# Performance work log

Hardware: AMD Instinct MI355X
Metric: run time of the kernel (lower is better)

The kernel has to match this reference:

```python
import jax, jax.numpy as jnp
import numpy as np

E, E2, T, C, H = 500_000, 1_000_000, 1_000_000, 64, 64
EPS, EPS2 = 0.0, 0.0  # train_eps=False, eps=eps2=0.0


def setup_inputs() -> dict:
    key = jax.random.key(0)
    ks = jax.random.split(key, 16)
    s = 1.0 / np.sqrt(C)
    return {
        "edge_attr": jax.random.normal(ks[0], (E, C), jnp.float32),
        "edge_attr2": jax.random.normal(ks[1], (E2, C), jnp.float32),
        # 6 projection layers (C -> C)
        "Wp": jax.random.normal(ks[2], (6, C, C), jnp.float32) * s,
        "bp": jnp.zeros((6, C), jnp.float32),
        # MLP 0 (for 1-hop edges): C -> H -> C
        "W1a": jax.random.normal(ks[3], (C, H), jnp.float32) * s,
        "b1a": jnp.zeros((H,), jnp.float32),
        "W2a": jax.random.normal(ks[4], (H, C), jnp.float32) * (1.0 / np.sqrt(H)),
        "b2a": jnp.zeros((C,), jnp.float32),
        # MLP 1 (for 2-hop edges): C -> H -> C
        "W1b": jax.random.normal(ks[5], (C, H), jnp.float32) * s,
        "b1b": jnp.zeros((H,), jnp.float32),
        "W2b": jax.random.normal(ks[6], (H, C), jnp.float32) * (1.0 / np.sqrt(H)),
        "b2b": jnp.zeros((C,), jnp.float32),
        # triangle index lists [3, T]; all values < E so valid for both edge arrays
        "triangle_1_1_1": jax.random.randint(ks[7], (3, T), 0, E, jnp.int64),
        "triangle_1_1_2": jax.random.randint(ks[8], (3, T), 0, E, jnp.int64),
        "triangle_1_2_2": jax.random.randint(ks[9], (3, T), 0, E, jnp.int64),
        "triangle_2_2_2": jax.random.randint(ks[10], (3, T), 0, E, jnp.int64),
        "inverse_edge_1": jax.random.randint(ks[11], (E,), 0, E, jnp.int64),
        "inverse_edge_2": jax.random.randint(ks[12], (E2,), 0, E, jnp.int64),
    }


def reference(edge_attr, edge_attr2, Wp, bp, W1a, b1a, W2a, b2a,
              W1b, b1b, W2b, b2b,
              triangle_1_1_1, triangle_1_1_2, triangle_1_2_2, triangle_2_2_2,
              inverse_edge_1, inverse_edge_2):
    num_edges = edge_attr.shape[0]
    num_edges2 = edge_attr2.shape[0]

    def proj(i, x):  # Linear proj i applied to gathered-sum features
        return x @ Wp[i] + bp[i]

    def mlp_a(x):
        return jax.nn.relu(x @ W1a + b1a) @ W2a + b2a

    def mlp_b(x):
        return jax.nn.relu(x @ W1b + b1b) @ W2b + b2b

    ij111, ik111, kj111 = triangle_1_1_1
    ij112, ik112, kj112 = triangle_1_1_2
    ij122, ik122, kj122 = triangle_1_2_2
    ij222, ik222, kj222 = triangle_2_2_2

    m111 = jax.ops.segment_sum(proj(0, edge_attr[ik111] + edge_attr[kj111]), ij111, num_segments=num_edges)
    m112 = jax.ops.segment_sum(proj(1, edge_attr[ik112] + edge_attr2[kj112]), ij112, num_segments=num_edges)
    m122 = jax.ops.segment_sum(proj(2, edge_attr2[ik122] + edge_attr2[kj122]), ij122, num_segments=num_edges)
    edge_attr = mlp_a(edge_attr * (1.0 + EPS) + m111 + m112 + m112[inverse_edge_1] + m122)

    m211 = jax.ops.segment_sum(proj(3, edge_attr[ij112] + edge_attr[ik112]), kj112, num_segments=num_edges2)
    m212 = jax.ops.segment_sum(proj(4, edge_attr[ij122] + edge_attr2[kj122]), ik122, num_segments=num_edges2)
    m222 = jax.ops.segment_sum(proj(5, edge_attr2[ik222] + edge_attr2[kj222]), ij222, num_segments=num_edges2)
    edge_attr2 = mlp_b(edge_attr2 * (1.0 + EPS2) + m211 + m212 + m212[inverse_edge_2] + m222)

    return (edge_attr, edge_attr2)
```

## Files before the change

kernel.cpp:

```cpp
#include <hip/hip_runtime.h>

#define CH 64
typedef unsigned int uint;
typedef unsigned short ushort;

typedef __attribute__((ext_vector_type(8))) short bf16x8;
typedef __attribute__((ext_vector_type(4))) float f32x4;

__device__ __forceinline__ float bf_lo(uint u){ union{uint a;float f;}c; c.a=u<<16; return c.f; }
__device__ __forceinline__ float bf_hi(uint u){ union{uint a;float f;}c; c.a=u&0xffff0000u; return c.f; }
__device__ __forceinline__ ushort f2bf(float f){
    uint a = __float_as_uint(f);
    a = (a + 0x7fffu + ((a>>16)&1u)) >> 16;
    return (ushort)a;
}
__device__ __forceinline__ uint pack2(float lo, float hi){
    return (uint)f2bf(lo) | ((uint)f2bf(hi) << 16);
}
__device__ __forceinline__ void atom_pk(uint* addr, float lo, float hi){
    uint v = pack2(lo, hi);
    asm volatile("global_atomic_pk_add_bf16 %0, %1, off" :: "v"(addr), "v"(v) : "memory");
}

template<bool ABF, bool BBF>
__global__ __launch_bounds__(256) void scatter_sum(
    const void* __restrict__ Av, const void* __restrict__ Bv,
    const int* __restrict__ idx_dst, const int* __restrict__ idx_a,
    const int* __restrict__ idx_b, int T,
    uint* __restrict__ S, float* __restrict__ cnt)
{
    const int l32  = threadIdx.x & 31;
    const int half = (threadIdx.x >> 5) & 1;
    const int wave  = blockIdx.x * (blockDim.x >> 6) + (threadIdx.x >> 6);
    const int nwave = gridDim.x * (blockDim.x >> 6);
    for (int w = wave; 2 * w < T; w += nwave) {
        const int t = 2 * w + half;
        if (t >= T) continue;
        const int ia = idx_a[t], ib = idx_b[t], id = idx_dst[t];
        float ax, ay, bx, by;
        if (ABF) { uint u = ((const uint*)Av)[(size_t)ia*32 + l32]; ax = bf_lo(u); ay = bf_hi(u); }
        else     { float2 v = ((const float2*)Av)[(size_t)ia*32 + l32]; ax = v.x; ay = v.y; }
        if (BBF) { uint u = ((const uint*)Bv)[(size_t)ib*32 + l32]; bx = bf_lo(u); by = bf_hi(u); }
        else     { float2 v = ((const float2*)Bv)[(size_t)ib*32 + l32]; bx = v.x; by = v.y; }
        atom_pk(S + (size_t)id*32 + l32, ax+bx, ay+by);
        if (l32 == 0) atomicAdd(&cnt[id], 1.0f);
    }
}

__global__ __launch_bounds__(256) void conv_bf16_kernel(
    const float* __restrict__ src, uint* __restrict__ dst, long n4)
{
    long i = (long)blockIdx.x * blockDim.x + threadIdx.x;
    const long stride = (long)gridDim.x * blockDim.x;
    for (; i < n4; i += stride) {
        const float4 v = ((const float4*)src)[i];
        uint2 o; o.x = pack2(v.x, v.y); o.y = pack2(v.z, v.w);
        ((uint2*)dst)[i] = o;
    }
}

struct W10 { const float* p[10]; };
__global__ __launch_bounds__(256) void prep_weights(W10 srcs, char* __restrict__ img)
{
    const float* W = srcs.p[blockIdx.x];
    char* im = img + (size_t)blockIdx.x * 8192;
    for (int idx = threadIdx.x; idx < 4096; idx += 256) {
        const int k = idx >> 6, col = idx & 63;
        *(ushort*)(im + col*128 + ((2*k) ^ ((col&7)<<4))) = f2bf(W[idx]);
    }
}

template<bool BASEBF>
__global__ __launch_bounds__(256) void fused_finalize_mfma(
    const void* __restrict__ base,
    const uint* __restrict__ SA, const float* __restrict__ cA,
    const uint* __restrict__ SB, const float* __restrict__ cB,
    const uint* __restrict__ SC, const float* __restrict__ cC,
    const int* __restrict__ inv,
    const char* __restrict__ wi0, const char* __restrict__ wi1,
    const char* __restrict__ wi2, const char* __restrict__ wi3,
    const char* __restrict__ wi4,
    const float* __restrict__ bA, const float* __restrict__ bB,
    const float* __restrict__ bC,
    const float* __restrict__ b1, const float* __restrict__ b2,
    int N, float* __restrict__ out, uint* __restrict__ out_bf)
{
    __shared__ __attribute__((aligned(16))) char lds[49152];
    const int tid = threadIdx.x;

    {
        const char* imgs[5] = {wi0, wi1, wi2, wi3, wi4};
        #pragma unroll
        for (int m = 0; m < 5; ++m) {
            const uint4* s = (const uint4*)imgs[m];
            uint4* d = (uint4*)(lds + m*8192);
            #pragma unroll
            for (int i = 0; i < 2; ++i) d[tid + 256*i] = s[tid + 256*i];
        }
    }
    __syncthreads();

    const int w = tid >> 6, lane = tid & 63;
    const int ln = lane & 15, grp = lane >> 4;
    char* zl = lds + 40960 + w * 2048;
    const int swz = (ln & 7) << 4;

    auto ldW = [&](int m, int kc, int ct) {
        const int col = ct*16 + ln;
        return *(const bf16x8*)(lds + m*8192 + col*128 + ((kc*64 + grp*16) ^ ((col&7)<<4)));
    };
    auto ldS = [&](const uint* Srow, int kc) {
        union { uint4 u; bf16x8 h; } c;
        c.u = *(const uint4*)(Srow + kc*16 + grp*4);
        return c.h;
    };
    auto ldZ = [&](int kc) {
        return *(const bf16x8*)(zl + ln*128 + ((kc*64 + grp*16) ^ swz));
    };
    auto stZ = [&](int ct, float v0, float v1, float v2, float v3) {
        uint2 u; u.x = pack2(v0, v1); u.y = pack2(v2, v3);
        *(uint2*)(zl + ln*128 + ((ct*32 + grp*8) ^ swz)) = u;
    };

    const f32x4 z4 = {0.f, 0.f, 0.f, 0.f};

    #pragma unroll 1
    for (int t = 0; t < 4; ++t) {
        const int rr = blockIdx.x * 256 + w * 64 + t * 16 + ln;
        const int ra = rr < N ? rr : N - 1;
        const bool valid = rr < N;
        const int iv = inv[ra];
        const float fA = cA[ra], fB = cB[ra], fC = cC[ra] + cC[iv];

        const uint* SArow  = SA + (size_t)ra * 32;
        const uint* SBrow  = SB + (size_t)ra * 32;
        const uint* SCrow  = SC + (size_t)ra * 32;
        const uint* SCrow2 = SC + (size_t)iv * 32;

        f32x4 acc[4] = {z4, z4, z4, z4};
        #pragma unroll
        for (int kc = 0; kc < 2; ++kc) {
            const bf16x8 sA = ldS(SArow, kc);
            const bf16x8 sB = ldS(SBrow, kc);
            const bf16x8 sC = ldS(SCrow, kc);
            const bf16x8 sD = ldS(SCrow2, kc);
            #pragma unroll
            for (int ct = 0; ct < 4; ++ct) {
                const bf16x8 wC = ldW(2, kc, ct);
                acc[ct] = __builtin_amdgcn_mfma_f32_16x16x32_bf16(ldW(0,kc,ct), sA, acc[ct], 0,0,0);
                acc[ct] = __builtin_amdgcn_mfma_f32_16x16x32_bf16(ldW(1,kc,ct), sB, acc[ct], 0,0,0);
                acc[ct] = __builtin_amdgcn_mfma_f32_16x16x32_bf16(wC,          sC, acc[ct], 0,0,0);
                acc[ct] = __builtin_amdgcn_mfma_f32_16x16x32_bf16(wC,          sD, acc[ct], 0,0,0);
            }
        }

        #pragma unroll
        for (int ct = 0; ct < 4; ++ct) {
            const int cb = ct*16 + grp*4;
            const float4 vA = *(const float4*)(bA + cb);
            const float4 vB = *(const float4*)(bB + cb);
            const float4 vC = *(const float4*)(bC + cb);
            float e0, e1, e2, e3;
            if (BASEBF) {
                const uint2 u = *(const uint2*)((const uint*)base + (size_t)ra*32 + (cb>>1));
                e0 = bf_lo(u.x); e1 = bf_hi(u.x); e2 = bf_lo(u.y); e3 = bf_hi(u.y);
            } else {
                const float4 b4 = *(const float4*)((const float*)base + (size_t)ra*64 + cb);
                e0 = b4.x; e1 = b4.y; e2 = b4.z; e3 = b4.w;
            }
            stZ(ct,
                acc[ct][0] + e0 + fA*vA.x + fB*vB.x + fC*vC.x,
                acc[ct][1] + e1 + fA*vA.y + fB*vB.y + fC*vC.y,
                acc[ct][2] + e2 + fA*vA.z + fB*vB.z + fC*vC.z,
                acc[ct][3] + e3 + fA*vA.w + fB*vB.w + fC*vC.w);
        }

        f32x4 hacc[4] = {z4, z4, z4, z4};
        #pragma unroll
        for (int kc = 0; kc < 2; ++kc) {
            const bf16x8 zf = ldZ(kc);
            #pragma unroll
            for (int ct = 0; ct < 4; ++ct)
                hacc[ct] = __builtin_amdgcn_mfma_f32_16x16x32_bf16(ldW(3,kc,ct), zf, hacc[ct], 0,0,0);
        }
        #pragma unroll
        for (int ct = 0; ct < 4; ++ct) {
            const int cb = ct*16 + grp*4;
            const float4 v1 = *(const float4*)(b1 + cb);
            stZ(ct, fmaxf(hacc[ct][0] + v1.x, 0.f), fmaxf(hacc[ct][1] + v1.y, 0.f),
                    fmaxf(hacc[ct][2] + v1.z, 0.f), fmaxf(hacc[ct][3] + v1.w, 0.f));
        }

        f32x4 oacc[4] = {z4, z4, z4, z4};
        #pragma unroll
        for (int kc = 0; kc < 2; ++kc) {
            const bf16x8 hf = ldZ(kc);
            #pragma unroll
            for (int ct = 0; ct < 4; ++ct)
                oacc[ct] = __builtin_amdgcn_mfma_f32_16x16x32_bf16(ldW(4,kc,ct), hf, oacc[ct], 0,0,0);
        }
        #pragma unroll
        for (int ct = 0; ct < 4; ++ct) {
            const int cb = ct*16 + grp*4;
            const float4 v2 = *(const float4*)(b2 + cb);
            const float o0 = oacc[ct][0] + v2.x, o1 = oacc[ct][1] + v2.y;
            const float o2 = oacc[ct][2] + v2.z, o3 = oacc[ct][3] + v2.w;
            if (valid) {
                *(float4*)(out + (size_t)ra*64 + cb) = make_float4(o0, o1, o2, o3);
                if (out_bf) {
                    uint2 u; u.x = pack2(o0, o1); u.y = pack2(o2, o3);
                    *(uint2*)(out_bf + (size_t)ra*32 + (cb>>1)) = u;
                }
            }
        }
    }
}

extern "C" void kernel_launch(void* const* d_in, const int* in_sizes, int n_in,
                              void* d_out, int out_size, void* d_ws, size_t ws_size,
                              hipStream_t stream)
{
    const float* ea  = (const float*)d_in[0];
    const float* ea2 = (const float*)d_in[1];
    const float* Wp  = (const float*)d_in[2];
    const float* bp  = (const float*)d_in[3];
    const float* W1a = (const float*)d_in[4];
    const float* b1a = (const float*)d_in[5];
    const float* W2a = (const float*)d_in[6];
    const float* b2a = (const float*)d_in[7];
    const float* W1b = (const float*)d_in[8];
    const float* b1b = (const float*)d_in[9];
    const float* W2b = (const float*)d_in[10];
    const float* b2b = (const float*)d_in[11];
    const int* t111 = (const int*)d_in[12];
    const int* t112 = (const int*)d_in[13];
    const int* t122 = (const int*)d_in[14];
    const int* t222 = (const int*)d_in[15];
    const int* inv1 = (const int*)d_in[16];
    const int* inv2 = (const int*)d_in[17];

    const int E    = in_sizes[0] / CH;
    const int E2   = in_sizes[1] / CH;
    const int T111 = in_sizes[12] / 3;
    const int T112 = in_sizes[13] / 3;
    const int T122 = in_sizes[14] / 3;
    const int T222 = in_sizes[15] / 3;

    float* out1 = (float*)d_out;
    float* out2 = out1 + (size_t)E * CH;

    const size_t R = (size_t)(E > E2 ? E : E2);
    char* p = (char*)d_ws;
    char*  Wimg = p;       p += 10 * 8192;
    uint*  SA = (uint*)p;  p += R * 128;
    uint*  SB = (uint*)p;  p += R * 128;
    uint*  SC = (uint*)p;  p += R * 128;
    float* cA = (float*)p; p += R * 4;
    float* cB = (float*)p; p += R * 4;
    float* cC = (float*)p; p += R * 4;
    size_t used = (size_t)(p - (char*)d_ws);
    uint* ea2_bf = nullptr;
    uint* ea_bf  = nullptr;
    uint* out1_bf = nullptr;
    if (ws_size >= used + (size_t)E2 * 128) { ea2_bf = (uint*)p; p += (size_t)E2 * 128; used += (size_t)E2 * 128; }
    if (ws_size >= used + (size_t)E  * 128) { ea_bf  = (uint*)p; p += (size_t)E  * 128; used += (size_t)E  * 128; }
    if (ws_size >= used + (size_t)E  * 128) { out1_bf = (uint*)p; }

    const dim3 blk256(256);
    const int SCAT_NB = 4096;

    auto scat = [&](const void* A, bool abf, const void* B, bool bbf,
                    const int* dst, const int* ia, const int* ib, int T,
                    uint* S, float* c) {
        if (abf && bbf)
            scatter_sum<true, true ><<<SCAT_NB, blk256, 0, stream>>>(A, B, dst, ia, ib, T, S, c);
        else if (abf)
            scatter_sum<true, false><<<SCAT_NB, blk256, 0, stream>>>(A, B, dst, ia, ib, T, S, c);
        else if (bbf)
            scatter_sum<false, true><<<SCAT_NB, blk256, 0, stream>>>(A, B, dst, ia, ib, T, S, c);
        else
            scatter_sum<false, false><<<SCAT_NB, blk256, 0, stream>>>(A, B, dst, ia, ib, T, S, c);
    };

    W10 w10;
    for (int i = 0; i < 6; ++i) w10.p[i] = Wp + (size_t)i * CH * CH;
    w10.p[6] = W1a; w10.p[7] = W2a; w10.p[8] = W1b; w10.p[9] = W2b;
    prep_weights<<<10, blk256, 0, stream>>>(w10, Wimg);

    if (ea2_bf) conv_bf16_kernel<<<2048, blk256, 0, stream>>>(ea2, ea2_bf, (long)E2 * 16);
    if (ea_bf)  conv_bf16_kernel<<<2048, blk256, 0, stream>>>(ea,  ea_bf,  (long)E  * 16);

    const void* eaS  = ea_bf  ? (const void*)ea_bf  : (const void*)ea;
    const void* ea2S = ea2_bf ? (const void*)ea2_bf : (const void*)ea2;
    const bool eaB = ea_bf != nullptr, ea2B = ea2_bf != nullptr;

    hipMemsetAsync(SA, 0, (size_t)E * 128, stream);
    hipMemsetAsync(SB, 0, (size_t)E * 128, stream);
    hipMemsetAsync(SC, 0, (size_t)E * 128, stream);
    hipMemsetAsync(cA, 0, (size_t)E * 4, stream);
    hipMemsetAsync(cB, 0, (size_t)E * 4, stream);
    hipMemsetAsync(cC, 0, (size_t)E * 4, stream);

    scat(eaS, eaB, eaS, eaB, t111 + 0, t111 + T111, t111 + 2*T111, T111, SA, cA);
    scat(ea2S, ea2B, ea2S, ea2B, t122 + 0, t122 + T122, t122 + 2*T122, T122, SB, cB);
    scat(eaS, eaB, ea2S, ea2B, t112 + 0, t112 + T112, t112 + 2*T112, T112, SC, cC);

    {
        const void* base1 = eaB ? (const void*)ea_bf : (const void*)ea;
        const int NB = (E + 255) / 256;
        if (eaB)
            fused_finalize_mfma<true><<<NB, blk256, 0, stream>>>(
                base1, SA, cA, SB, cB, SC, cC, inv1,
                Wimg + 0*8192, Wimg + 2*8192, Wimg + 1*8192, Wimg + 6*8192, Wimg + 7*8192,
                bp + 0*CH, bp + 2*CH, bp + 1*CH, b1a, b2a, E, out1, out1_bf);
        else
            fused_finalize_mfma<false><<<NB, blk256, 0, stream>>>(
                base1, SA, cA, SB, cB, SC, cC, inv1,
                Wimg + 0*8192, Wimg + 2*8192, Wimg + 1*8192, Wimg + 6*8192, Wimg + 7*8192,
                bp + 0*CH, bp + 2*CH, bp + 1*CH, b1a, b2a, E, out1, out1_bf);
    }

    hipMemsetAsync(SA, 0, (size_t)E2 * 128, stream);
    hipMemsetAsync(SB, 0, (size_t)E2 * 128, stream);
    hipMemsetAsync(SC, 0, (size_t)E2 * 128, stream);
    hipMemsetAsync(cA, 0, (size_t)E2 * 4, stream);
    hipMemsetAsync(cB, 0, (size_t)E2 * 4, stream);
    hipMemsetAsync(cC, 0, (size_t)E2 * 4, stream);

    const void* o1S = out1_bf ? (const void*)out1_bf : (const void*)out1;
    const bool o1B = out1_bf != nullptr;

    scat(o1S, o1B, o1S, o1B, t112 + 2*T112, t112 + 0, t112 + T112, T112, SA, cA);
    scat(ea2S, ea2B, ea2S, ea2B, t222 + 0, t222 + T222, t222 + 2*T222, T222, SB, cB);
    scat(o1S, o1B, ea2S, ea2B, t122 + T122, t122 + 0, t122 + 2*T122, T122, SC, cC);

    {
        const void* base2 = ea2B ? (const void*)ea2_bf : (const void*)ea2;
        const int NB = (E2 + 255) / 256;
        if (ea2B)
            fused_finalize_mfma<true><<<NB, blk256, 0, stream>>>(
                base2, SA, cA, SB, cB, SC, cC, inv2,
                Wimg + 3*8192, Wimg + 5*8192, Wimg + 4*8192, Wimg + 8*8192, Wimg + 9*8192,
                bp + 3*CH, bp + 5*CH, bp + 4*CH, b1b, b2b, E2, out2, nullptr);
        else
            fused_finalize_mfma<false><<<NB, blk256, 0, stream>>>(
                base2, SA, cA, SB, cB, SC, cC, inv2,
                Wimg + 3*8192, Wimg + 5*8192, Wimg + 4*8192, Wimg + 8*8192, Wimg + 9*8192,
                bp + 3*CH, bp + 5*CH, bp + 4*CH, b1b, b2b, E2, out2, nullptr);
    }
}
```

Measured before the change: 1.765 ms.

## Split fused finalize into projection-sum and MLP kernels to cut LDS per block

```diff
diff --git a/kernel.cpp b/kernel.cpp
--- a/kernel.cpp
+++ b/kernel.cpp
@@ -71,27 +71,24 @@
 }
 
 template<bool BASEBF>
-__global__ __launch_bounds__(256) void fused_finalize_mfma(
+__global__ __launch_bounds__(256, 4) void proj_sum_mfma(
     const void* __restrict__ base,
     const uint* __restrict__ SA, const float* __restrict__ cA,
     const uint* __restrict__ SB, const float* __restrict__ cB,
     const uint* __restrict__ SC, const float* __restrict__ cC,
     const int* __restrict__ inv,
-    const char* __restrict__ wi0, const char* __restrict__ wi1,
-    const char* __restrict__ wi2, const char* __restrict__ wi3,
-    const char* __restrict__ wi4,
+    const char* __restrict__ wiA, const char* __restrict__ wiB,
+    const char* __restrict__ wiC,
     const float* __restrict__ bA, const float* __restrict__ bB,
     const float* __restrict__ bC,
-    const float* __restrict__ b1, const float* __restrict__ b2,
-    int N, float* __restrict__ out, uint* __restrict__ out_bf)
-{
-    __shared__ __attribute__((aligned(16))) char lds[49152];
+    int N, uint* __restrict__ z)
+{
+    __shared__ __attribute__((aligned(16))) char lds[24576];
     const int tid = threadIdx.x;
-
     {
-        const char* imgs[5] = {wi0, wi1, wi2, wi3, wi4};
-        #pragma unroll
-        for (int m = 0; m < 5; ++m) {
+        const char* imgs[3] = {wiA, wiB, wiC};
+        #pragma unroll
+        for (int m = 0; m < 3; ++m) {
             const uint4* s = (const uint4*)imgs[m];
             uint4* d = (uint4*)(lds + m*8192);
             #pragma unroll
@@ -102,8 +99,6 @@
 
     const int w = tid >> 6, lane = tid & 63;
     const int ln = lane & 15, grp = lane >> 4;
-    char* zl = lds + 40960 + w * 2048;
-    const int swz = (ln & 7) << 4;
 
     auto ldW = [&](int m, int kc, int ct) {
         const int col = ct*16 + ln;
@@ -113,13 +108,6 @@
         union { uint4 u; bf16x8 h; } c;
         c.u = *(const uint4*)(Srow + kc*16 + grp*4);
         return c.h;
-    };
-    auto ldZ = [&](int kc) {
-        return *(const bf16x8*)(zl + ln*128 + ((kc*64 + grp*16) ^ swz));
-    };
-    auto stZ = [&](int ct, float v0, float v1, float v2, float v3) {
-        uint2 u; u.x = pack2(v0, v1); u.y = pack2(v2, v3);
-        *(uint2*)(zl + ln*128 + ((ct*32 + grp*8) ^ swz)) = u;
     };
 
     const f32x4 z4 = {0.f, 0.f, 0.f, 0.f};
@@ -168,36 +156,92 @@
                 const float4 b4 = *(const float4*)((const float*)base + (size_t)ra*64 + cb);
                 e0 = b4.x; e1 = b4.y; e2 = b4.z; e3 = b4.w;
             }
-            stZ(ct,
-                acc[ct][0] + e0 + fA*vA.x + fB*vB.x + fC*vC.x,
-                acc[ct][1] + e1 + fA*vA.y + fB*vB.y + fC*vC.y,
-                acc[ct][2] + e2 + fA*vA.z + fB*vB.z + fC*vC.z,
-                acc[ct][3] + e3 + fA*vA.w + fB*vB.w + fC*vC.w);
-        }
+            if (valid) {
+                uint2 u;
+                u.x = pack2(acc[ct][0] + e0 + fA*vA.x + fB*vB.x + fC*vC.x,
+                            acc[ct][1] + e1 + fA*vA.y + fB*vB.y + fC*vC.y);
+                u.y = pack2(acc[ct][2] + e2 + fA*vA.z + fB*vB.z + fC*vC.z,
+                            acc[ct][3] + e3 + fA*vA.w + fB*vB.w + fC*vC.w);
+                *(uint2*)(z + (size_t)ra*32 + (cb>>1)) = u;
+            }
+        }
+    }
+}
+
+__global__ __launch_bounds__(256, 4) void mlp_mfma(
+    const uint* __restrict__ z,
+    const char* __restrict__ wi1, const char* __restrict__ wi2,
+    const float* __restrict__ b1, const float* __restrict__ b2,
+    int N, float* __restrict__ out, uint* __restrict__ out_bf)
+{
+    __shared__ __attribute__((aligned(16))) char lds[24576];
+    const int tid = threadIdx.x;
+    {
+        const char* imgs[2] = {wi1, wi2};
+        #pragma unroll
+        for (int m = 0; m < 2; ++m) {
+            const uint4* s = (const uint4*)imgs[m];
+            uint4* d = (uint4*)(lds + m*8192);
+            #pragma unroll
+            for (int i = 0; i < 2; ++i) d[tid + 256*i] = s[tid + 256*i];
+        }
+    }
+    __syncthreads();
+
+    const int w = tid >> 6, lane = tid & 63;
+    const int ln = lane & 15, grp = lane >> 4;
+    char* zl = lds + 16384 + w * 2048;
+    const int swz = (ln & 7) << 4;
+
+    auto ldW = [&](int m, int kc, int ct) {
+        const int col = ct*16 + ln;
+        return *(const bf16x8*)(lds + m*8192 + col*128 + ((kc*64 + grp*16) ^ ((col&7)<<4)));
+    };
+    auto ldZg = [&](const uint* zrow, int kc) {
+        union { uint4 u; bf16x8 h; } c;
+        c.u = *(const uint4*)(zrow + kc*16 + grp*4);
+        return c.h;
+    };
+    auto ldZl = [&](int kc) {
+        return *(const bf16x8*)(zl + ln*128 + ((kc*64 + grp*16) ^ swz));
+    };
+    auto stZl = [&](int ct, float v0, float v1, float v2, float v3) {
+        uint2 u; u.x = pack2(v0, v1); u.y = pack2(v2, v3);
+        *(uint2*)(zl + ln*128 + ((ct*32 + grp*8) ^ swz)) = u;
+    };
+
+    const f32x4 z4 = {0.f, 0.f, 0.f, 0.f};
+
+    #pragma unroll 1
+    for (int t = 0; t < 4; ++t) {
+        const int rr = blockIdx.x * 256 + w * 64 + t * 16 + ln;
+        const int ra = rr < N ? rr : N - 1;
+        const bool valid = rr < N;
+        const uint* zrow = z + (size_t)ra * 32;
 
         f32x4 hacc[4] = {z4, z4, z4, z4};
         #pragma unroll
         for (int kc = 0; kc < 2; ++kc) {
-            const bf16x8 zf = ldZ(kc);
+            const bf16x8 zf = ldZg(zrow, kc);
             #pragma unroll
             for (int ct = 0; ct < 4; ++ct)
-                hacc[ct] = __builtin_amdgcn_mfma_f32_16x16x32_bf16(ldW(3,kc,ct), zf, hacc[ct], 0,0,0);
+                hacc[ct] = __builtin_amdgcn_mfma_f32_16x16x32_bf16(ldW(0,kc,ct), zf, hacc[ct], 0,0,0);
         }
         #pragma unroll
         for (int ct = 0; ct < 4; ++ct) {
             const int cb = ct*16 + grp*4;
             const float4 v1 = *(const float4*)(b1 + cb);
-            stZ(ct, fmaxf(hacc[ct][0] + v1.x, 0.f), fmaxf(hacc[ct][1] + v1.y, 0.f),
-                    fmaxf(hacc[ct][2] + v1.z, 0.f), fmaxf(hacc[ct][3] + v1.w, 0.f));
+            stZl(ct, fmaxf(hacc[ct][0] + v1.x, 0.f), fmaxf(hacc[ct][1] + v1.y, 0.f),
+                     fmaxf(hacc[ct][2] + v1.z, 0.f), fmaxf(hacc[ct][3] + v1.w, 0.f));
         }
 
         f32x4 oacc[4] = {z4, z4, z4, z4};
         #pragma unroll
         for (int kc = 0; kc < 2; ++kc) {
-            const bf16x8 hf = ldZ(kc);
+            const bf16x8 hf = ldZl(kc);
             #pragma unroll
             for (int ct = 0; ct < 4; ++ct)
-                oacc[ct] = __builtin_amdgcn_mfma_f32_16x16x32_bf16(ldW(4,kc,ct), hf, oacc[ct], 0,0,0);
+                oacc[ct] = __builtin_amdgcn_mfma_f32_16x16x32_bf16(ldW(1,kc,ct), hf, oacc[ct], 0,0,0);
         }
         #pragma unroll
         for (int ct = 0; ct < 4; ++ct) {
@@ -258,13 +302,14 @@
     float* cA = (float*)p; p += R * 4;
     float* cB = (float*)p; p += R * 4;
     float* cC = (float*)p; p += R * 4;
+    uint*  zbuf = (uint*)p; p += R * 128;
     size_t used = (size_t)(p - (char*)d_ws);
     uint* ea2_bf = nullptr;
+    uint* out1_bf = nullptr;
     uint* ea_bf  = nullptr;
-    uint* out1_bf = nullptr;
     if (ws_size >= used + (size_t)E2 * 128) { ea2_bf = (uint*)p; p += (size_t)E2 * 128; used += (size_t)E2 * 128; }
-    if (ws_size >= used + (size_t)E  * 128) { ea_bf  = (uint*)p; p += (size_t)E  * 128; used += (size_t)E  * 128; }
-    if (ws_size >= used + (size_t)E  * 128) { out1_bf = (uint*)p; }
+    if (ws_size >= used + (size_t)E  * 128) { out1_bf = (uint*)p; p += (size_t)E * 128; used += (size_t)E * 128; }
+    if (ws_size >= used + (size_t)E  * 128) { ea_bf  = (uint*)p; }
 
     const dim3 blk256(256);
     const int SCAT_NB = 4096;
@@ -306,18 +351,19 @@
     scat(eaS, eaB, ea2S, ea2B, t112 + 0, t112 + T112, t112 + 2*T112, T112, SC, cC);
 
     {
-        const void* base1 = eaB ? (const void*)ea_bf : (const void*)ea;
         const int NB = (E + 255) / 256;
         if (eaB)
-            fused_finalize_mfma<true><<<NB, blk256, 0, stream>>>(
-                base1, SA, cA, SB, cB, SC, cC, inv1,
-                Wimg + 0*8192, Wimg + 2*8192, Wimg + 1*8192, Wimg + 6*8192, Wimg + 7*8192,
-                bp + 0*CH, bp + 2*CH, bp + 1*CH, b1a, b2a, E, out1, out1_bf);
+            proj_sum_mfma<true><<<NB, blk256, 0, stream>>>(
+                (const void*)ea_bf, SA, cA, SB, cB, SC, cC, inv1,
+                Wimg + 0*8192, Wimg + 2*8192, Wimg + 1*8192,
+                bp + 0*CH, bp + 2*CH, bp + 1*CH, E, zbuf);
         else
-            fused_finalize_mfma<false><<<NB, blk256, 0, stream>>>(
-                base1, SA, cA, SB, cB, SC, cC, inv1,
-                Wimg + 0*8192, Wimg + 2*8192, Wimg + 1*8192, Wimg + 6*8192, Wimg + 7*8192,
-                bp + 0*CH, bp + 2*CH, bp + 1*CH, b1a, b2a, E, out1, out1_bf);
+            proj_sum_mfma<false><<<NB, blk256, 0, stream>>>(
+                (const void*)ea, SA, cA, SB, cB, SC, cC, inv1,
+                Wimg + 0*8192, Wimg + 2*8192, Wimg + 1*8192,
+                bp + 0*CH, bp + 2*CH, bp + 1*CH, E, zbuf);
+        mlp_mfma<<<NB, blk256, 0, stream>>>(
+            zbuf, Wimg + 6*8192, Wimg + 7*8192, b1a, b2a, E, out1, out1_bf);
     }
 
     hipMemsetAsync(SA, 0, (size_t)E2 * 128, stream);
@@ -335,17 +381,18 @@
     scat(o1S, o1B, ea2S, ea2B, t122 + T122, t122 + 0, t122 + 2*T122, T122, SC, cC);
 
     {
-        const void* base2 = ea2B ? (const void*)ea2_bf : (const void*)ea2;
         const int NB = (E2 + 255) / 256;
         if (ea2B)
-            fused_finalize_mfma<true><<<NB, blk256, 0, stream>>>(
-                base2, SA, cA, SB, cB, SC, cC, inv2,
-                Wimg + 3*8192, Wimg + 5*8192, Wimg + 4*8192, Wimg + 8*8192, Wimg + 9*8192,
-                bp + 3*CH, bp + 5*CH, bp + 4*CH, b1b, b2b, E2, out2, nullptr);
+            proj_sum_mfma<true><<<NB, blk256, 0, stream>>>(
+                (const void*)ea2_bf, SA, cA, SB, cB, SC, cC, inv2,
+                Wimg + 3*8192, Wimg + 5*8192, Wimg + 4*8192,
+                bp + 3*CH, bp + 5*CH, bp + 4*CH, E2, zbuf);
         else
-            fused_finalize_mfma<false><<<NB, blk256, 0, stream>>>(
-                base2, SA, cA, SB, cB, SC, cC, inv2,
-                Wimg + 3*8192, Wimg + 5*8192, Wimg + 4*8192, Wimg + 8*8192, Wimg + 9*8192,
-                bp + 3*CH, bp + 5*CH, bp + 4*CH, b1b, b2b, E2, out2, nullptr);
-    }
-}
+            proj_sum_mfma<false><<<NB, blk256, 0, stream>>>(
+                (const void*)ea2, SA, cA, SB, cB, SC, cC, inv2,
+                Wimg + 3*8192, Wimg + 5*8192, Wimg + 4*8192,
+                bp + 3*CH, bp + 5*CH, bp + 4*CH, E2, zbuf);
+        mlp_mfma<<<NB, blk256, 0, stream>>>(
+            zbuf, Wimg + 8*8192, Wimg + 9*8192, b1b, b2b, E2, out2, nullptr);
+    }
+}
```

Result: slower. 1.886 ms (+6.9%).

## Merge three scatter launches into one multi-job kernel and widen finalize blocks

Applied to the files above, without the earlier changes.

```diff
diff --git a/kernel.cpp b/kernel.cpp
--- a/kernel.cpp
+++ b/kernel.cpp
@@ -22,26 +22,37 @@
     asm volatile("global_atomic_pk_add_bf16 %0, %1, off" :: "v"(addr), "v"(v) : "memory");
 }
 
-template<bool ABF, bool BBF>
-__global__ __launch_bounds__(256) void scatter_sum(
-    const void* __restrict__ Av, const void* __restrict__ Bv,
-    const int* __restrict__ idx_dst, const int* __restrict__ idx_a,
-    const int* __restrict__ idx_b, int T,
-    uint* __restrict__ S, float* __restrict__ cnt)
-{
+struct ScatJobs {
+    const void* A[3]; const void* B[3];
+    const int* dst[3]; const int* ia[3]; const int* ib[3];
+    uint* S[3]; float* cnt[3];
+    int T[3]; int abf[3]; int bbf[3];
+};
+__global__ __launch_bounds__(256) void scatter3(ScatJobs J)
+{
+    const int job = blockIdx.x % 3;
+    const int bj  = blockIdx.x / 3;
+    const int nbj = gridDim.x / 3;
     const int l32  = threadIdx.x & 31;
     const int half = (threadIdx.x >> 5) & 1;
-    const int wave  = blockIdx.x * (blockDim.x >> 6) + (threadIdx.x >> 6);
-    const int nwave = gridDim.x * (blockDim.x >> 6);
+    const int wave = bj * 4 + (threadIdx.x >> 6);
+    const int nwave = nbj * 4;
+
+    const void* A = J.A[job]; const void* B = J.B[job];
+    const int* idst = J.dst[job]; const int* iia = J.ia[job]; const int* iib = J.ib[job];
+    uint* S = J.S[job]; float* cnt = J.cnt[job];
+    const int T = J.T[job];
+    const bool abf = J.abf[job] != 0, bbf = J.bbf[job] != 0;
+
     for (int w = wave; 2 * w < T; w += nwave) {
         const int t = 2 * w + half;
         if (t >= T) continue;
-        const int ia = idx_a[t], ib = idx_b[t], id = idx_dst[t];
+        const int ia = iia[t], ib = iib[t], id = idst[t];
         float ax, ay, bx, by;
-        if (ABF) { uint u = ((const uint*)Av)[(size_t)ia*32 + l32]; ax = bf_lo(u); ay = bf_hi(u); }
-        else     { float2 v = ((const float2*)Av)[(size_t)ia*32 + l32]; ax = v.x; ay = v.y; }
-        if (BBF) { uint u = ((const uint*)Bv)[(size_t)ib*32 + l32]; bx = bf_lo(u); by = bf_hi(u); }
-        else     { float2 v = ((const float2*)Bv)[(size_t)ib*32 + l32]; bx = v.x; by = v.y; }
+        if (abf) { uint u = ((const uint*)A)[(size_t)ia*32 + l32]; ax = bf_lo(u); ay = bf_hi(u); }
+        else     { float2 v = ((const float2*)A)[(size_t)ia*32 + l32]; ax = v.x; ay = v.y; }
+        if (bbf) { uint u = ((const uint*)B)[(size_t)ib*32 + l32]; bx = bf_lo(u); by = bf_hi(u); }
+        else     { float2 v = ((const float2*)B)[(size_t)ib*32 + l32]; bx = v.x; by = v.y; }
         atom_pk(S + (size_t)id*32 + l32, ax+bx, ay+by);
         if (l32 == 0) atomicAdd(&cnt[id], 1.0f);
     }
@@ -71,32 +82,28 @@
 }
 
 template<bool BASEBF>
-__global__ __launch_bounds__(256) void fused_finalize_mfma(
+__global__ __launch_bounds__(512, 4) void fused_finalize_mfma(
     const void* __restrict__ base,
     const uint* __restrict__ SA, const float* __restrict__ cA,
     const uint* __restrict__ SB, const float* __restrict__ cB,
     const uint* __restrict__ SC, const float* __restrict__ cC,
     const int* __restrict__ inv,
-    const char* __restrict__ wi0, const char* __restrict__ wi1,
-    const char* __restrict__ wi2, const char* __restrict__ wi3,
-    const char* __restrict__ wi4,
+    const char* __restrict__ wiA, const char* __restrict__ wiB,
+    const char* __restrict__ wiC, const char* __restrict__ wi1,
+    const char* __restrict__ wi2,
     const float* __restrict__ bA, const float* __restrict__ bB,
     const float* __restrict__ bC,
     const float* __restrict__ b1, const float* __restrict__ b2,
     int N, float* __restrict__ out, uint* __restrict__ out_bf)
 {
-    __shared__ __attribute__((aligned(16))) char lds[49152];
+    __shared__ __attribute__((aligned(16))) char lds[57344];
     const int tid = threadIdx.x;
 
     {
-        const char* imgs[5] = {wi0, wi1, wi2, wi3, wi4};
-        #pragma unroll
-        for (int m = 0; m < 5; ++m) {
-            const uint4* s = (const uint4*)imgs[m];
-            uint4* d = (uint4*)(lds + m*8192);
-            #pragma unroll
-            for (int i = 0; i < 2; ++i) d[tid + 256*i] = s[tid + 256*i];
-        }
+        const char* imgs[5] = {wiA, wiB, wiC, wi1, wi2};
+        #pragma unroll
+        for (int m = 0; m < 5; ++m)
+            ((uint4*)(lds + m*8192))[tid] = ((const uint4*)imgs[m])[tid];
     }
     __syncthreads();
 
@@ -114,10 +121,10 @@
         c.u = *(const uint4*)(Srow + kc*16 + grp*4);
         return c.h;
     };
-    auto ldZ = [&](int kc) {
+    auto ldZl = [&](int kc) {
         return *(const bf16x8*)(zl + ln*128 + ((kc*64 + grp*16) ^ swz));
     };
-    auto stZ = [&](int ct, float v0, float v1, float v2, float v3) {
+    auto stZl = [&](int ct, float v0, float v1, float v2, float v3) {
         uint2 u; u.x = pack2(v0, v1); u.y = pack2(v2, v3);
         *(uint2*)(zl + ln*128 + ((ct*32 + grp*8) ^ swz)) = u;
     };
@@ -125,8 +132,8 @@
     const f32x4 z4 = {0.f, 0.f, 0.f, 0.f};
 
     #pragma unroll 1
-    for (int t = 0; t < 4; ++t) {
-        const int rr = blockIdx.x * 256 + w * 64 + t * 16 + ln;
+    for (int t = 0; t < 2; ++t) {
+        const int rr = blockIdx.x * 256 + w * 32 + t * 16 + ln;
         const int ra = rr < N ? rr : N - 1;
         const bool valid = rr < N;
         const int iv = inv[ra];
@@ -168,17 +175,17 @@
                 const float4 b4 = *(const float4*)((const float*)base + (size_t)ra*64 + cb);
                 e0 = b4.x; e1 = b4.y; e2 = b4.z; e3 = b4.w;
             }
-            stZ(ct,
-                acc[ct][0] + e0 + fA*vA.x + fB*vB.x + fC*vC.x,
-                acc[ct][1] + e1 + fA*vA.y + fB*vB.y + fC*vC.y,
-                acc[ct][2] + e2 + fA*vA.z + fB*vB.z + fC*vC.z,
-                acc[ct][3] + e3 + fA*vA.w + fB*vB.w + fC*vC.w);
+            stZl(ct,
+                 acc[ct][0] + e0 + fA*vA.x + fB*vB.x + fC*vC.x,
+                 acc[ct][1] + e1 + fA*vA.y + fB*vB.y + fC*vC.y,
+                 acc[ct][2] + e2 + fA*vA.z + fB*vB.z + fC*vC.z,
+                 acc[ct][3] + e3 + fA*vA.w + fB*vB.w + fC*vC.w);
         }
 
         f32x4 hacc[4] = {z4, z4, z4, z4};
         #pragma unroll
         for (int kc = 0; kc < 2; ++kc) {
-            const bf16x8 zf = ldZ(kc);
+            const bf16x8 zf = ldZl(kc);
             #pragma unroll
             for (int ct = 0; ct < 4; ++ct)
                 hacc[ct] = __builtin_amdgcn_mfma_f32_16x16x32_bf16(ldW(3,kc,ct), zf, hacc[ct], 0,0,0);
@@ -187,14 +194,14 @@
         for (int ct = 0; ct < 4; ++ct) {
             const int cb = ct*16 + grp*4;
             const float4 v1 = *(const float4*)(b1 + cb);
-            stZ(ct, fmaxf(hacc[ct][0] + v1.x, 0.f), fmaxf(hacc[ct][1] + v1.y, 0.f),
-                    fmaxf(hacc[ct][2] + v1.z, 0.f), fmaxf(hacc[ct][3] + v1.w, 0.f));
+            stZl(ct, fmaxf(hacc[ct][0] + v1.x, 0.f), fmaxf(hacc[ct][1] + v1.y, 0.f),
+                     fmaxf(hacc[ct][2] + v1.z, 0.f), fmaxf(hacc[ct][3] + v1.w, 0.f));
         }
 
         f32x4 oacc[4] = {z4, z4, z4, z4};
         #pragma unroll
         for (int kc = 0; kc < 2; ++kc) {
-            const bf16x8 hf = ldZ(kc);
+            const bf16x8 hf = ldZl(kc);
             #pragma unroll
             for (int ct = 0; ct < 4; ++ct)
                 oacc[ct] = __builtin_amdgcn_mfma_f32_16x16x32_bf16(ldW(4,kc,ct), hf, oacc[ct], 0,0,0);
@@ -260,27 +267,14 @@
     float* cC = (float*)p; p += R * 4;
     size_t used = (size_t)(p - (char*)d_ws);
     uint* ea2_bf = nullptr;
+    uint* out1_bf = nullptr;
     uint* ea_bf  = nullptr;
-    uint* out1_bf = nullptr;
     if (ws_size >= used + (size_t)E2 * 128) { ea2_bf = (uint*)p; p += (size_t)E2 * 128; used += (size_t)E2 * 128; }
-    if (ws_size >= used + (size_t)E  * 128) { ea_bf  = (uint*)p; p += (size_t)E  * 128; used += (size_t)E  * 128; }
-    if (ws_size >= used + (size_t)E  * 128) { out1_bf = (uint*)p; }
-
-    const dim3 blk256(256);
-    const int SCAT_NB = 4096;
-
-    auto scat = [&](const void* A, bool abf, const void* B, bool bbf,
-                    const int* dst, const int* ia, const int* ib, int T,
-                    uint* S, float* c) {
-        if (abf && bbf)
-            scatter_sum<true, true ><<<SCAT_NB, blk256, 0, stream>>>(A, B, dst, ia, ib, T, S, c);
-        else if (abf)
-            scatter_sum<true, false><<<SCAT_NB, blk256, 0, stream>>>(A, B, dst, ia, ib, T, S, c);
-        else if (bbf)
-            scatter_sum<false, true><<<SCAT_NB, blk256, 0, stream>>>(A, B, dst, ia, ib, T, S, c);
-        else
-            scatter_sum<false, false><<<SCAT_NB, blk256, 0, stream>>>(A, B, dst, ia, ib, T, S, c);
-    };
+    if (ws_size >= used + (size_t)E  * 128) { out1_bf = (uint*)p; p += (size_t)E * 128; used += (size_t)E * 128; }
+    if (ws_size >= used + (size_t)E  * 128) { ea_bf  = (uint*)p; }
+
+    const dim3 blk256(256), blk512(512);
+    const int SCAT3_NB = 12288;
 
     W10 w10;
     for (int i = 0; i < 6; ++i) w10.p[i] = Wp + (size_t)i * CH * CH;
@@ -292,7 +286,7 @@
 
     const void* eaS  = ea_bf  ? (const void*)ea_bf  : (const void*)ea;
     const void* ea2S = ea2_bf ? (const void*)ea2_bf : (const void*)ea2;
-    const bool eaB = ea_bf != nullptr, ea2B = ea2_bf != nullptr;
+    const int eaB = ea_bf != nullptr, ea2B = ea2_bf != nullptr;
 
     hipMemsetAsync(SA, 0, (size_t)E * 128, stream);
     hipMemsetAsync(SB, 0, (size_t)E * 128, stream);
@@ -301,21 +295,27 @@
     hipMemsetAsync(cB, 0, (size_t)E * 4, stream);
     hipMemsetAsync(cC, 0, (size_t)E * 4, stream);
 
-    scat(eaS, eaB, eaS, eaB, t111 + 0, t111 + T111, t111 + 2*T111, T111, SA, cA);
-    scat(ea2S, ea2B, ea2S, ea2B, t122 + 0, t122 + T122, t122 + 2*T122, T122, SB, cB);
-    scat(eaS, eaB, ea2S, ea2B, t112 + 0, t112 + T112, t112 + 2*T112, T112, SC, cC);
-
-    {
-        const void* base1 = eaB ? (const void*)ea_bf : (const void*)ea;
+    {
+        ScatJobs J;
+        J.A[0]=eaS;  J.B[0]=eaS;  J.dst[0]=t111+0;      J.ia[0]=t111+T111; J.ib[0]=t111+2*T111;
+        J.S[0]=SA; J.cnt[0]=cA; J.T[0]=T111; J.abf[0]=eaB;  J.bbf[0]=eaB;
+        J.A[1]=ea2S; J.B[1]=ea2S; J.dst[1]=t122+0;      J.ia[1]=t122+T122; J.ib[1]=t122+2*T122;
+        J.S[1]=SB; J.cnt[1]=cB; J.T[1]=T122; J.abf[1]=ea2B; J.bbf[1]=ea2B;
+        J.A[2]=eaS;  J.B[2]=ea2S; J.dst[2]=t112+0;      J.ia[2]=t112+T112; J.ib[2]=t112+2*T112;
+        J.S[2]=SC; J.cnt[2]=cC; J.T[2]=T112; J.abf[2]=eaB;  J.bbf[2]=ea2B;
+        scatter3<<<SCAT3_NB, blk256, 0, stream>>>(J);
+    }
+
+    {
         const int NB = (E + 255) / 256;
         if (eaB)
-            fused_finalize_mfma<true><<<NB, blk256, 0, stream>>>(
-                base1, SA, cA, SB, cB, SC, cC, inv1,
+            fused_finalize_mfma<true><<<NB, blk512, 0, stream>>>(
+                (const void*)ea_bf, SA, cA, SB, cB, SC, cC, inv1,
                 Wimg + 0*8192, Wimg + 2*8192, Wimg + 1*8192, Wimg + 6*8192, Wimg + 7*8192,
                 bp + 0*CH, bp + 2*CH, bp + 1*CH, b1a, b2a, E, out1, out1_bf);
         else
-            fused_finalize_mfma<false><<<NB, blk256, 0, stream>>>(
-                base1, SA, cA, SB, cB, SC, cC, inv1,
+            fused_finalize_mfma<false><<<NB, blk512, 0, stream>>>(
+                (const void*)ea, SA, cA, SB, cB, SC, cC, inv1,
                 Wimg + 0*8192, Wimg + 2*8192, Wimg + 1*8192, Wimg + 6*8192, Wimg + 7*8192,
                 bp + 0*CH, bp + 2*CH, bp + 1*CH, b1a, b2a, E, out1, out1_bf);
     }
@@ -328,23 +328,29 @@
     hipMemsetAsync(cC, 0, (size_t)E2 * 4, stream);
 
     const void* o1S = out1_bf ? (const void*)out1_bf : (const void*)out1;
-    const bool o1B = out1_bf != nullptr;
-
-    scat(o1S, o1B, o1S, o1B, t112 + 2*T112, t112 + 0, t112 + T112, T112, SA, cA);
-    scat(ea2S, ea2B, ea2S, ea2B, t222 + 0, t222 + T222, t222 + 2*T222, T222, SB, cB);
-    scat(o1S, o1B, ea2S, ea2B, t122 + T122, t122 + 0, t122 + 2*T122, T122, SC, cC);
-
-    {
-        const void* base2 = ea2B ? (const void*)ea2_bf : (const void*)ea2;
+    const int o1B = out1_bf != nullptr;
+
+    {
+        ScatJobs J;
+        J.A[0]=o1S;  J.B[0]=o1S;  J.dst[0]=t112+2*T112; J.ia[0]=t112+0;    J.ib[0]=t112+T112;
+        J.S[0]=SA; J.cnt[0]=cA; J.T[0]=T112; J.abf[0]=o1B;  J.bbf[0]=o1B;
+        J.A[1]=ea2S; J.B[1]=ea2S; J.dst[1]=t222+0;      J.ia[1]=t222+T222; J.ib[1]=t222+2*T222;
+        J.S[1]=SB; J.cnt[1]=cB; J.T[1]=T222; J.abf[1]=ea2B; J.bbf[1]=ea2B;
+        J.A[2]=o1S;  J.B[2]=ea2S; J.dst[2]=t122+T122;   J.ia[2]=t122+0;    J.ib[2]=t122+2*T122;
+        J.S[2]=SC; J.cnt[2]=cC; J.T[2]=T122; J.abf[2]=o1B;  J.bbf[2]=ea2B;
+        scatter3<<<SCAT3_NB, blk256, 0, stream>>>(J);
+    }
+
+    {
         const int NB = (E2 + 255) / 256;
         if (ea2B)
-            fused_finalize_mfma<true><<<NB, blk256, 0, stream>>>(
-                base2, SA, cA, SB, cB, SC, cC, inv2,
+            fused_finalize_mfma<true><<<NB, blk512, 0, stream>>>(
+                (const void*)ea2_bf, SA, cA, SB, cB, SC, cC, inv2,
                 Wimg + 3*8192, Wimg + 5*8192, Wimg + 4*8192, Wimg + 8*8192, Wimg + 9*8192,
                 bp + 3*CH, bp + 5*CH, bp + 4*CH, b1b, b2b, E2, out2, nullptr);
         else
-            fused_finalize_mfma<false><<<NB, blk256, 0, stream>>>(
-                base2, SA, cA, SB, cB, SC, cC, inv2,
+            fused_finalize_mfma<false><<<NB, blk512, 0, stream>>>(
+                (const void*)ea2, SA, cA, SB, cB, SC, cC, inv2,
                 Wimg + 3*8192, Wimg + 5*8192, Wimg + 4*8192, Wimg + 8*8192, Wimg + 9*8192,
                 bp + 3*CH, bp + 5*CH, bp + 4*CH, b1b, b2b, E2, out2, nullptr);
     }
```

New measurement: 2.906 ms. 64.6% more time.
